# Performance work log

Hardware: AMD Instinct MI355X
Metric: run time of the kernel (lower is better)

Reference implementation:

```python
import jax, jax.numpy as jnp
import numpy as np

D_MODEL = 1024
NHEAD = 16
HEAD_DIM = D_MODEL // NHEAD
LN_EPS = 1e-5
ROPE_BASE = 10000.0


def _rope_cos_sin(n, head_dim):
    inv_freq = 1.0 / (ROPE_BASE ** (jnp.arange(0, head_dim, 2, dtype=jnp.float32) / head_dim))
    t = jnp.arange(n, dtype=jnp.float32)
    freqs = jnp.outer(t, inv_freq)  # (N, head_dim//2)
    return jnp.cos(freqs), jnp.sin(freqs)


def _apply_rope(x, cos, sin):
    # x: (B, H, N, hd); cos/sin: (N, hd//2)
    B, H, N, hd = x.shape
    xr = x.reshape(B, H, N, hd // 2, 2)
    x0, x1 = xr[..., 0], xr[..., 1]
    c = cos[None, None]
    s = sin[None, None]
    rot = jnp.stack([x0 * c - x1 * s, x0 * s + x1 * c], axis=-1)
    return rot.reshape(B, H, N, hd)


def setup_inputs() -> dict:
    key = jax.random.key(0)
    ks = jax.random.split(key, 6)
    D = D_MODEL
    scale = 1.0 / np.sqrt(D)
    x = jax.random.normal(ks[0], (2, 2048, D), dtype=jnp.float32)
    Wq = jax.random.normal(ks[1], (D, D), dtype=jnp.float32) * scale
    Wk = jax.random.normal(ks[2], (D, D), dtype=jnp.float32) * scale
    Wv = jax.random.normal(ks[3], (D, D), dtype=jnp.float32) * scale
    Wo = jax.random.normal(ks[4], (D, D), dtype=jnp.float32) * scale
    bq = jnp.zeros((D,), jnp.float32)
    bk = jnp.zeros((D,), jnp.float32)
    bv = jnp.zeros((D,), jnp.float32)
    bo = jnp.zeros((D,), jnp.float32)
    ln_w = jnp.ones((D,), jnp.float32)
    ln_b = jnp.zeros((D,), jnp.float32)
    return {"x": x, "ln_w": ln_w, "ln_b": ln_b, "Wq": Wq, "bq": bq,
            "Wk": Wk, "bk": bk, "Wv": Wv, "bv": bv, "Wo": Wo, "bo": bo}


def reference(x, ln_w, ln_b, Wq, bq, Wk, bk, Wv, bv, Wo, bo):
    B, N, D = x.shape
    H, hd = NHEAD, HEAD_DIM
    # LayerNorm
    mu = jnp.mean(x, axis=-1, keepdims=True)
    var = jnp.mean(jnp.square(x - mu), axis=-1, keepdims=True)
    xn = (x - mu) * jax.lax.rsqrt(var + LN_EPS) * ln_w + ln_b
    # QKV projections -> (B, H, N, hd)
    def proj(W, b):
        return (xn @ W.T + b).reshape(B, N, H, hd).transpose(0, 2, 1, 3)
    q = proj(Wq, bq)
    k = proj(Wk, bk)
    v = proj(Wv, bv)
    cos, sin = _rope_cos_sin(N, hd)
    q = _apply_rope(q, cos, sin)
    k = _apply_rope(k, cos, sin)
    scores = jnp.einsum('bhqd,bhkd->bhqk', q, k) / jnp.sqrt(jnp.float32(hd))
    attn = jax.nn.softmax(scores, axis=-1)
    out = jnp.einsum('bhqk,bhkd->bhqd', attn, v)
    out = out.transpose(0, 2, 1, 3).reshape(B, N, D)
    return x + out @ Wo.T + bo
```

## Files before the change

### kernel.cpp

```cpp
#include <hip/hip_runtime.h>


#define SEQ 2048
#define LN_EPS 1e-5f

using short8 = __attribute__((ext_vector_type(8))) short;
using f32x4  = __attribute__((ext_vector_type(4))) float;

__device__ __forceinline__ unsigned short f2bf(float f) {
  union { float f; unsigned u; } v; v.f = f;
  unsigned r = v.u + 0x7FFFu + ((v.u >> 16) & 1u);
  return (unsigned short)(r >> 16);
}

__device__ __forceinline__ void async16(const void* g, void* l) {
  __builtin_amdgcn_global_load_lds(
      (const __attribute__((address_space(1))) void*)g,
      (__attribute__((address_space(3))) void*)l, 16, 0, 0);
}

__global__ __launch_bounds__(256) void prep_kernel(
    const float* __restrict__ x, const float* __restrict__ lnw, const float* __restrict__ lnb,
    const float* __restrict__ wq, const float* __restrict__ wk,
    const float* __restrict__ wv, const float* __restrict__ wo,
    unsigned short* __restrict__ wqkv, unsigned short* __restrict__ wob,
    unsigned short* __restrict__ xn, float2* __restrict__ tab) {
  const int b = blockIdx.x, t = threadIdx.x;
  if (b < 4096) {
    const int gid = b * 256 + t;
    const int m = gid >> 18, e4 = gid & 262143;
    const float* src = (m == 0) ? wq : (m == 1) ? wk : (m == 2) ? wv : wo;
    const float4 v = ((const float4*)src)[e4];
    ushort4 o; o.x = f2bf(v.x); o.y = f2bf(v.y); o.z = f2bf(v.z); o.w = f2bf(v.w);
    if (m < 3) ((ushort4*)wqkv)[(size_t)m * 262144 + e4] = o;
    else       ((ushort4*)wob)[e4] = o;
  } else if (b < 8192) {
    const int row = b - 4096;
    const float4 v = ((const float4*)(x + (size_t)row * 1024))[t];
    float s  = v.x + v.y + v.z + v.w;
    float s2 = v.x * v.x + v.y * v.y + v.z * v.z + v.w * v.w;
#pragma unroll
    for (int off = 32; off >= 1; off >>= 1) {
      s  += __shfl_xor(s, off);
      s2 += __shfl_xor(s2, off);
    }
    __shared__ float red[8];
    const int lane = t & 63, wave = t >> 6;
    if (lane == 0) { red[wave] = s; red[4 + wave] = s2; }
    __syncthreads();
    s  = red[0] + red[1] + red[2] + red[3];
    s2 = red[4] + red[5] + red[6] + red[7];
    const float mu   = s * (1.0f / 1024.0f);
    const float var  = s2 * (1.0f / 1024.0f) - mu * mu;
    const float rstd = rsqrtf(var + LN_EPS);
    const float4 wv4 = ((const float4*)lnw)[t];
    const float4 bv4 = ((const float4*)lnb)[t];
    ushort4 o;
    o.x = f2bf((v.x - mu) * rstd * wv4.x + bv4.x);
    o.y = f2bf((v.y - mu) * rstd * wv4.y + bv4.y);
    o.z = f2bf((v.z - mu) * rstd * wv4.z + bv4.z);
    o.w = f2bf((v.w - mu) * rstd * wv4.w + bv4.w);
    ((ushort4*)xn)[(size_t)row * 256 + t] = o;
  } else {
    const int gid = (b - 8192) * 256 + t;
    const int pos = gid >> 5, ip = gid & 31;
    const float invf = exp2f((float)ip * -0.4152410118609203f);
    const float fr = (float)pos * invf;
    tab[gid] = make_float2(cosf(fr), sinf(fr));
  }
}

__global__ __launch_bounds__(256, 3) void gemm_qkv_kernel(
    const unsigned short* __restrict__ A,
    const unsigned short* __restrict__ Bw,
    const float* __restrict__ bq, const float* __restrict__ bk, const float* __restrict__ bv,
    const float2* __restrict__ tab,
    unsigned short* __restrict__ qb, unsigned short* __restrict__ kbg,
    unsigned short* __restrict__ vtb) {
  __shared__ unsigned short lA[128 * 64];
  __shared__ unsigned short lB[128 * 64];
  const int tid = threadIdx.x;
  const int lane = tid & 63, wave = tid >> 6;
  const int lr = lane & 15, quad = lane >> 4;
  const int wm = (wave >> 1) * 64, wn = (wave & 1) * 64;
  const int n0 = blockIdx.x * 128, m0 = blockIdx.y * 128;
  const int r7 = lr & 7;
  const int lrow = lane >> 3, lcg = (lane & 7) ^ lrow;
  const int lin = blockIdx.y * gridDim.x + blockIdx.x;
  const int phase = ((lin >> 8) * 5) & 15;

  f32x4 acc[4][4];
#pragma unroll
  for (int i = 0; i < 4; ++i)
#pragma unroll
    for (int j = 0; j < 4; ++j) acc[i][j] = (f32x4){0.f, 0.f, 0.f, 0.f};

  for (int kt = 0; kt < 16; ++kt) {
    const int kofs = ((kt + phase) & 15) * 64;
    __syncthreads();
#pragma unroll
    for (int c = 0; c < 4; ++c) {
      const int chunk = wave * 4 + c;
      const int grow = chunk * 8 + lrow;
      async16(&A[(size_t)(m0 + grow) * 1024 + kofs + lcg * 8], &lA[chunk * 512]);
      async16(&Bw[(size_t)(n0 + grow) * 1024 + kofs + lcg * 8], &lB[chunk * 512]);
    }
    __syncthreads();
#pragma unroll
    for (int kk = 0; kk < 2; ++kk) {
      short8 a[4], b[4];
#pragma unroll
      for (int i = 0; i < 4; ++i)
        a[i] = *(const short8*)&lA[(wm + i * 16 + lr) * 64 + ((kk * 4 + quad) ^ r7) * 8];
#pragma unroll
      for (int j = 0; j < 4; ++j)
        b[j] = *(const short8*)&lB[(wn + j * 16 + lr) * 64 + ((kk * 4 + quad) ^ r7) * 8];
#pragma unroll
      for (int i = 0; i < 4; ++i)
#pragma unroll
        for (int j = 0; j < 4; ++j)
          acc[i][j] = __builtin_amdgcn_mfma_f32_16x16x32_bf16(a[i], b[j], acc[i][j], 0, 0, 0);
    }
  }

  const int which = n0 >> 10;
  const float* bias = (which == 0) ? bq : (which == 1) ? bk : bv;
  const float qs = (which == 0) ? 0.18033688011112042f : 1.0f;
#pragma unroll
  for (int i = 0; i < 4; ++i)
#pragma unroll
    for (int j = 0; j < 4; ++j)
#pragma unroll
      for (int r = 0; r < 4; ++r) {
        const int row = m0 + wm + i * 16 + quad * 4 + r;
        const int col = n0 + wn + j * 16 + lr;
        const int c = col & 1023;
        float val = (acc[i][j][r] + bias[c]) * qs;
        const int head = c >> 6, hd_i = c & 63;
        const int b_ = row >> 11, pos = row & 2047;
        if (which < 2) {
          const float partner = __shfl_xor(val, 1);
          const float2 cs = tab[(pos << 5) + (hd_i >> 1)];
          val = val * cs.x + partner * ((lane & 1) ? cs.y : -cs.y);
        }
        if (which == 2) {
          vtb[((size_t)((b_ * 16 + head) * 64 + hd_i)) * SEQ + pos] = f2bf(val);
        } else {
          const size_t didx = ((size_t)((b_ * 16 + head) * SEQ + pos)) * 64 + hd_i;
          if (which == 0) qb[didx] = f2bf(val);
          else            kbg[didx] = f2bf(val);
        }
      }
}

__global__ __launch_bounds__(256, 3) void gemm_o_kernel(
    const unsigned short* __restrict__ A,
    const unsigned short* __restrict__ Bw,
    const float* __restrict__ bo, const float* __restrict__ xres, float* __restrict__ out) {
  __shared__ unsigned short lA[128 * 64];
  __shared__ unsigned short lB[64 * 64];
  const int tid = threadIdx.x;
  const int lane = tid & 63, wave = tid >> 6;
  const int lr = lane & 15, quad = lane >> 4;
  const int wm = (wave >> 1) * 64, wn = (wave & 1) * 32;
  const int n0 = blockIdx.x * 64, m0 = blockIdx.y * 128;
  const int r7 = lr & 7;
  const int lrow = lane >> 3, lcg = (lane & 7) ^ lrow;
  const int lin = blockIdx.y * gridDim.x + blockIdx.x;
  const int phase = ((lin >> 8) * 8) & 15;

  f32x4 acc[4][2];
#pragma unroll
  for (int i = 0; i < 4; ++i)
#pragma unroll
    for (int j = 0; j < 2; ++j) acc[i][j] = (f32x4){0.f, 0.f, 0.f, 0.f};

  for (int kt = 0; kt < 16; ++kt) {
    const int kofs = ((kt + phase) & 15) * 64;
    __syncthreads();
#pragma unroll
    for (int c = 0; c < 4; ++c) {
      const int chunk = wave * 4 + c;
      const int grow = chunk * 8 + lrow;
      async16(&A[(size_t)(m0 + grow) * 1024 + kofs + lcg * 8], &lA[chunk * 512]);
    }
#pragma unroll
    for (int c = 0; c < 2; ++c) {
      const int chunk = wave * 2 + c;
      const int grow = chunk * 8 + lrow;
      async16(&Bw[(size_t)(n0 + grow) * 1024 + kofs + lcg * 8], &lB[chunk * 512]);
    }
    __syncthreads();
#pragma unroll
    for (int kk = 0; kk < 2; ++kk) {
      short8 a[4], b[2];
#pragma unroll
      for (int i = 0; i < 4; ++i)
        a[i] = *(const short8*)&lA[(wm + i * 16 + lr) * 64 + ((kk * 4 + quad) ^ r7) * 8];
#pragma unroll
      for (int j = 0; j < 2; ++j)
        b[j] = *(const short8*)&lB[(wn + j * 16 + lr) * 64 + ((kk * 4 + quad) ^ r7) * 8];
#pragma unroll
      for (int i = 0; i < 4; ++i)
#pragma unroll
        for (int j = 0; j < 2; ++j)
          acc[i][j] = __builtin_amdgcn_mfma_f32_16x16x32_bf16(a[i], b[j], acc[i][j], 0, 0, 0);
    }
  }

#pragma unroll
  for (int i = 0; i < 4; ++i)
#pragma unroll
    for (int j = 0; j < 2; ++j)
#pragma unroll
      for (int r = 0; r < 4; ++r) {
        const int row = m0 + wm + i * 16 + quad * 4 + r;
        const int col = n0 + wn + j * 16 + lr;
        const size_t idx = (size_t)row * 1024 + col;
        out[idx] = acc[i][j][r] + bo[col] + xres[idx];
      }
}

__global__ __launch_bounds__(256) void attn_kernel(
    const unsigned short* __restrict__ qg, const unsigned short* __restrict__ kg,
    const unsigned short* __restrict__ vtg, unsigned short* __restrict__ ao) {
  __shared__ unsigned short lK[128 * 64];
  __shared__ unsigned short lV[64 * 128];
  __shared__ unsigned short lP[4][32 * 128];
  const int tid = threadIdx.x;
  const int lane = tid & 63, w = tid >> 6;
  const int lr = lane & 15, quad = lane >> 4;
  const int r7 = lr & 7;
  const int bh = blockIdx.x >> 4, qt = blockIdx.x & 15;
  const int q0 = qt * 128 + w * 32;
  const int phase = ((blockIdx.x >> 8) * 8) & 15;
  const unsigned short* Q  = qg + (size_t)bh * SEQ * 64;
  const unsigned short* K  = kg + (size_t)bh * SEQ * 64;
  const unsigned short* VT = vtg + (size_t)bh * 64 * SEQ;
  unsigned short* lPw = lP[w];

  short8 qf[2][2];
#pragma unroll
  for (int t = 0; t < 2; ++t)
#pragma unroll
    for (int kk = 0; kk < 2; ++kk)
      qf[t][kk] = *(const short8*)&Q[(size_t)(q0 + t * 16 + lr) * 64 + kk * 32 + quad * 8];

  short8 onesf;
  {
    const short o1 = (lr == 0) ? (short)0x3F80 : (short)0;
#pragma unroll
    for (int j = 0; j < 8; ++j) onesf[j] = o1;
  }

  f32x4 o[2][4], ol[2];
#pragma unroll
  for (int t = 0; t < 2; ++t) {
    ol[t] = (f32x4){0.f, 0.f, 0.f, 0.f};
#pragma unroll
    for (int d = 0; d < 4; ++d) o[t][d] = (f32x4){0.f, 0.f, 0.f, 0.f};
  }

  const int k_row = lane >> 3, k_g = (lane & 7) ^ (k_row & 7);
  const int v_row = lane >> 4, v_g0 = lane & 15;

  for (int kt = 0; kt < 16; ++kt) {
    const int kb0 = ((kt + phase) & 15) * 128;
    __syncthreads();
#pragma unroll
    for (int c = 0; c < 4; ++c) {
      const int kc = w * 4 + c;
      const int krow = kc * 8 + k_row;
      async16(&K[(size_t)(kb0 + krow) * 64 + k_g * 8], &lK[kc * 512]);
      const int vc = w * 4 + c;
      const int vrow = vc * 4 + v_row;
      const int vg = v_g0 ^ (vrow & 7);
      async16(&VT[(size_t)vrow * SEQ + kb0 + vg * 8], &lV[vc * 512]);
    }
    __syncthreads();

#pragma unroll
    for (int kb = 0; kb < 8; ++kb) {
      const short8 k0 = *(const short8*)&lK[(kb * 16 + lr) * 64 + (quad ^ r7) * 8];
      const short8 k1 = *(const short8*)&lK[(kb * 16 + lr) * 64 + ((4 + quad) ^ r7) * 8];
#pragma unroll
      for (int t = 0; t < 2; ++t) {
        f32x4 st = (f32x4){0.f, 0.f, 0.f, 0.f};
        st = __builtin_amdgcn_mfma_f32_16x16x32_bf16(k0, qf[t][0], st, 0, 0, 0);
        st = __builtin_amdgcn_mfma_f32_16x16x32_bf16(k1, qf[t][1], st, 0, 0, 0);
        union { float f; unsigned u; } c0, c1, c2, c3;
        c0.f = __builtin_amdgcn_exp2f(st[0]);
        c1.f = __builtin_amdgcn_exp2f(st[1]);
        c2.f = __builtin_amdgcn_exp2f(st[2]);
        c3.f = __builtin_amdgcn_exp2f(st[3]);
        uint2 pw;
        pw.x = __builtin_amdgcn_perm(c1.u, c0.u, 0x07060302u);
        pw.y = __builtin_amdgcn_perm(c3.u, c2.u, 0x07060302u);
        *(uint2*)&lPw[(t * 16 + lr) * 128 + ((kb * 2 + (quad >> 1)) ^ r7) * 8 + (quad & 1) * 4] = pw;
      }
    }
    __asm__ __volatile__("s_waitcnt lgkmcnt(0)" ::: "memory");

#pragma unroll
    for (int k2 = 0; k2 < 4; ++k2) {
      const short8 pf0 = *(const short8*)&lPw[lr * 128 + ((k2 * 4 + quad) ^ r7) * 8];
      const short8 pf1 = *(const short8*)&lPw[(16 + lr) * 128 + ((k2 * 4 + quad) ^ r7) * 8];
      ol[0] = __builtin_amdgcn_mfma_f32_16x16x32_bf16(pf0, onesf, ol[0], 0, 0, 0);
      ol[1] = __builtin_amdgcn_mfma_f32_16x16x32_bf16(pf1, onesf, ol[1], 0, 0, 0);
#pragma unroll
      for (int d = 0; d < 4; ++d) {
        const short8 vf = *(const short8*)&lV[(d * 16 + lr) * 128 + ((k2 * 4 + quad) ^ r7) * 8];
        o[0][d] = __builtin_amdgcn_mfma_f32_16x16x32_bf16(pf0, vf, o[0][d], 0, 0, 0);
        o[1][d] = __builtin_amdgcn_mfma_f32_16x16x32_bf16(pf1, vf, o[1][d], 0, 0, 0);
      }
    }
  }

  const int b_ = bh >> 4, h = bh & 15;
#pragma unroll
  for (int t = 0; t < 2; ++t)
#pragma unroll
    for (int r = 0; r < 4; ++r) {
      const float l = __shfl(ol[t][r], lane & 48);
      const float rl = 1.0f / l;
#pragma unroll
      for (int d = 0; d < 4; ++d) {
        const int row = q0 + t * 16 + quad * 4 + r;
        ao[(size_t)(b_ * SEQ + row) * 1024 + h * 64 + d * 16 + lr] = f2bf(o[t][d][r] * rl);
      }
    }
}

extern "C" void kernel_launch(void* const* d_in, const int* in_sizes, int n_in,
                              void* d_out, int out_size, void* d_ws, size_t ws_size,
                              hipStream_t stream) {
  const float* x   = (const float*)d_in[0];
  const float* lnw = (const float*)d_in[1];
  const float* lnb = (const float*)d_in[2];
  const float* Wq  = (const float*)d_in[3];
  const float* bq  = (const float*)d_in[4];
  const float* Wk  = (const float*)d_in[5];
  const float* bk  = (const float*)d_in[6];
  const float* Wv  = (const float*)d_in[7];
  const float* bv  = (const float*)d_in[8];
  const float* Wo  = (const float*)d_in[9];
  const float* bo  = (const float*)d_in[10];
  float* out = (float*)d_out;

  char* ws = (char*)d_ws;
  unsigned short* wqkv = (unsigned short*)(ws);
  unsigned short* wob  = (unsigned short*)(ws + 6291456);
  unsigned short* xn   = (unsigned short*)(ws + 8388608);
  unsigned short* qb   = (unsigned short*)(ws + 16777216);
  unsigned short* kbuf = (unsigned short*)(ws + 25165824);
  unsigned short* vtb  = (unsigned short*)(ws + 33554432);
  unsigned short* ao   = (unsigned short*)(ws + 41943040);
  float2*         tab  = (float2*)(ws + 50331648);

  hipLaunchKernelGGL(prep_kernel, dim3(8448), dim3(256), 0, stream,
                     x, lnw, lnb, Wq, Wk, Wv, Wo, wqkv, wob, xn, tab);
  hipLaunchKernelGGL(gemm_qkv_kernel, dim3(24, 32), dim3(256), 0, stream,
                     xn, wqkv, bq, bk, bv, tab, qb, kbuf, vtb);
  hipLaunchKernelGGL(attn_kernel, dim3(512), dim3(256), 0, stream, qb, kbuf, vtb, ao);
  hipLaunchKernelGGL(gemm_o_kernel, dim3(16, 32), dim3(256), 0, stream,
                     ao, wob, bo, x, out);
}
```

Before: 220.8 us.

## Rewrite attention with 32x32 MFMA, register-resident P, and double-buffered K/V

The attention kernel moves from 16x16x32 to 32x32x16 bf16 MFMA tiles. Probabilities stay in registers, rearranged with permlane32_swap, instead of round-tripping through per-wave LDS. The row sum is accumulated with scalar adds rather than a ones-vector MFMA. K/V tiles are double-buffered so the next tile's async loads overlap compute, which drops one barrier per iteration. This doubles the K/V LDS footprint and adds cross-lane shuffles, and correctness depends on matching the 32x32 accumulator layout.

Result: no change. 223.9 us (+1.4%).

```diff
diff --git a/kernel.cpp b/kernel.cpp
--- a/kernel.cpp
+++ b/kernel.cpp
@@ -6,6 +6,7 @@
 
 using short8 = __attribute__((ext_vector_type(8))) short;
 using f32x4  = __attribute__((ext_vector_type(4))) float;
+using f32x16 = __attribute__((ext_vector_type(16))) float;
 
 __device__ __forceinline__ unsigned short f2bf(float f) {
   union { float f; unsigned u; } v; v.f = f;
@@ -224,111 +225,125 @@
 __global__ __launch_bounds__(256) void attn_kernel(
     const unsigned short* __restrict__ qg, const unsigned short* __restrict__ kg,
     const unsigned short* __restrict__ vtg, unsigned short* __restrict__ ao) {
-  __shared__ unsigned short lK[128 * 64];
-  __shared__ unsigned short lV[64 * 128];
-  __shared__ unsigned short lP[4][32 * 128];
+  __shared__ unsigned short lK[2][128 * 64];
+  __shared__ unsigned short lV[2][64 * 128];
   const int tid = threadIdx.x;
   const int lane = tid & 63, w = tid >> 6;
-  const int lr = lane & 15, quad = lane >> 4;
-  const int r7 = lr & 7;
+  const int l31 = lane & 31, hb = lane >> 5, l7 = lane & 7;
   const int bh = blockIdx.x >> 4, qt = blockIdx.x & 15;
-  const int q0 = qt * 128 + w * 32;
+  const int q0w = qt * 128 + w * 32;
   const int phase = ((blockIdx.x >> 8) * 8) & 15;
   const unsigned short* Q  = qg + (size_t)bh * SEQ * 64;
   const unsigned short* K  = kg + (size_t)bh * SEQ * 64;
   const unsigned short* VT = vtg + (size_t)bh * 64 * SEQ;
-  unsigned short* lPw = lP[w];
-
-  short8 qf[2][2];
-#pragma unroll
-  for (int t = 0; t < 2; ++t)
-#pragma unroll
-    for (int kk = 0; kk < 2; ++kk)
-      qf[t][kk] = *(const short8*)&Q[(size_t)(q0 + t * 16 + lr) * 64 + kk * 32 + quad * 8];
-
-  short8 onesf;
-  {
-    const short o1 = (lr == 0) ? (short)0x3F80 : (short)0;
-#pragma unroll
-    for (int j = 0; j < 8; ++j) onesf[j] = o1;
-  }
-
-  f32x4 o[2][4], ol[2];
-#pragma unroll
-  for (int t = 0; t < 2; ++t) {
-    ol[t] = (f32x4){0.f, 0.f, 0.f, 0.f};
-#pragma unroll
-    for (int d = 0; d < 4; ++d) o[t][d] = (f32x4){0.f, 0.f, 0.f, 0.f};
-  }
+
+  short8 qf[4];
+#pragma unroll
+  for (int c = 0; c < 4; ++c)
+    qf[c] = *(const short8*)&Q[(size_t)(q0w + l31) * 64 + c * 16 + hb * 8];
+
+  f32x16 o[2];
+#pragma unroll
+  for (int dh = 0; dh < 2; ++dh)
+#pragma unroll
+    for (int r = 0; r < 16; ++r) o[dh][r] = 0.f;
+  float ls = 0.f;
 
   const int k_row = lane >> 3, k_g = (lane & 7) ^ (k_row & 7);
   const int v_row = lane >> 4, v_g0 = lane & 15;
 
-  for (int kt = 0; kt < 16; ++kt) {
-    const int kb0 = ((kt + phase) & 15) * 128;
-    __syncthreads();
+  {
+    const int kb0 = (phase & 15) * 128;
 #pragma unroll
     for (int c = 0; c < 4; ++c) {
       const int kc = w * 4 + c;
       const int krow = kc * 8 + k_row;
-      async16(&K[(size_t)(kb0 + krow) * 64 + k_g * 8], &lK[kc * 512]);
-      const int vc = w * 4 + c;
-      const int vrow = vc * 4 + v_row;
+      async16(&K[(size_t)(kb0 + krow) * 64 + k_g * 8], &lK[0][kc * 512]);
+      const int vrow = kc * 4 + v_row;
       const int vg = v_g0 ^ (vrow & 7);
-      async16(&VT[(size_t)vrow * SEQ + kb0 + vg * 8], &lV[vc * 512]);
-    }
-    __syncthreads();
-
-#pragma unroll
-    for (int kb = 0; kb < 8; ++kb) {
-      const short8 k0 = *(const short8*)&lK[(kb * 16 + lr) * 64 + (quad ^ r7) * 8];
-      const short8 k1 = *(const short8*)&lK[(kb * 16 + lr) * 64 + ((4 + quad) ^ r7) * 8];
-#pragma unroll
-      for (int t = 0; t < 2; ++t) {
-        f32x4 st = (f32x4){0.f, 0.f, 0.f, 0.f};
-        st = __builtin_amdgcn_mfma_f32_16x16x32_bf16(k0, qf[t][0], st, 0, 0, 0);
-        st = __builtin_amdgcn_mfma_f32_16x16x32_bf16(k1, qf[t][1], st, 0, 0, 0);
-        union { float f; unsigned u; } c0, c1, c2, c3;
-        c0.f = __builtin_amdgcn_exp2f(st[0]);
-        c1.f = __builtin_amdgcn_exp2f(st[1]);
-        c2.f = __builtin_amdgcn_exp2f(st[2]);
-        c3.f = __builtin_amdgcn_exp2f(st[3]);
-        uint2 pw;
-        pw.x = __builtin_amdgcn_perm(c1.u, c0.u, 0x07060302u);
-        pw.y = __builtin_amdgcn_perm(c3.u, c2.u, 0x07060302u);
-        *(uint2*)&lPw[(t * 16 + lr) * 128 + ((kb * 2 + (quad >> 1)) ^ r7) * 8 + (quad & 1) * 4] = pw;
-      }
-    }
-    __asm__ __volatile__("s_waitcnt lgkmcnt(0)" ::: "memory");
-
-#pragma unroll
-    for (int k2 = 0; k2 < 4; ++k2) {
-      const short8 pf0 = *(const short8*)&lPw[lr * 128 + ((k2 * 4 + quad) ^ r7) * 8];
-      const short8 pf1 = *(const short8*)&lPw[(16 + lr) * 128 + ((k2 * 4 + quad) ^ r7) * 8];
-      ol[0] = __builtin_amdgcn_mfma_f32_16x16x32_bf16(pf0, onesf, ol[0], 0, 0, 0);
-      ol[1] = __builtin_amdgcn_mfma_f32_16x16x32_bf16(pf1, onesf, ol[1], 0, 0, 0);
-#pragma unroll
-      for (int d = 0; d < 4; ++d) {
-        const short8 vf = *(const short8*)&lV[(d * 16 + lr) * 128 + ((k2 * 4 + quad) ^ r7) * 8];
-        o[0][d] = __builtin_amdgcn_mfma_f32_16x16x32_bf16(pf0, vf, o[0][d], 0, 0, 0);
-        o[1][d] = __builtin_amdgcn_mfma_f32_16x16x32_bf16(pf1, vf, o[1][d], 0, 0, 0);
-      }
-    }
-  }
+      async16(&VT[(size_t)vrow * SEQ + kb0 + vg * 8], &lV[0][kc * 512]);
+    }
+  }
+  __syncthreads();
+
+  for (int kt = 0; kt < 16; ++kt) {
+    const int cur = kt & 1;
+    if (kt < 15) {
+      const int kb0 = ((kt + 1 + phase) & 15) * 128;
+#pragma unroll
+      for (int c = 0; c < 4; ++c) {
+        const int kc = w * 4 + c;
+        const int krow = kc * 8 + k_row;
+        async16(&K[(size_t)(kb0 + krow) * 64 + k_g * 8], &lK[cur ^ 1][kc * 512]);
+        const int vrow = kc * 4 + v_row;
+        const int vg = v_g0 ^ (vrow & 7);
+        async16(&VT[(size_t)vrow * SEQ + kb0 + vg * 8], &lV[cur ^ 1][kc * 512]);
+      }
+    }
+    const unsigned short* Kb = lK[cur];
+    const unsigned short* Vb = lV[cur];
+
+#pragma unroll
+    for (int kb2 = 0; kb2 < 4; ++kb2) {
+      f32x16 sv;
+#pragma unroll
+      for (int r = 0; r < 16; ++r) sv[r] = 0.f;
+      const int key = kb2 * 32 + l31;
+#pragma unroll
+      for (int c = 0; c < 4; ++c) {
+        const short8 af = *(const short8*)&Kb[key * 64 + (((c * 2 + hb) ^ l7) << 3)];
+        sv = __builtin_amdgcn_mfma_f32_32x32x16_bf16(af, qf[c], sv, 0, 0, 0);
+      }
+      unsigned wp[8];
+#pragma unroll
+      for (int p = 0; p < 8; ++p) {
+        union { float f; unsigned u; } e0, e1;
+        e0.f = __builtin_amdgcn_exp2f(sv[2 * p]);
+        e1.f = __builtin_amdgcn_exp2f(sv[2 * p + 1]);
+        ls += e0.f + e1.f;
+        wp[p] = __builtin_amdgcn_perm(e1.u, e0.u, 0x07060302u);
+      }
+      unsigned wlo[8], whi[8];
+#pragma unroll
+      for (int p = 0; p < 8; ++p) {
+        auto rr = __builtin_amdgcn_permlane32_swap(wp[p], wp[p], false, false);
+        wlo[p] = rr[0]; whi[p] = rr[1];
+      }
+#pragma unroll
+      for (int cl = 0; cl < 2; ++cl) {
+        const int pb = cl * 4;
+        union { unsigned u[4]; short8 s; } pf;
+        pf.u[0] = hb ? wlo[pb + 2] : wlo[pb + 0];
+        pf.u[1] = hb ? wlo[pb + 3] : wlo[pb + 1];
+        pf.u[2] = hb ? whi[pb + 2] : whi[pb + 0];
+        pf.u[3] = hb ? whi[pb + 3] : whi[pb + 1];
+        const int chunk = kb2 * 2 + cl;
+#pragma unroll
+        for (int dh = 0; dh < 2; ++dh) {
+          const int d = dh * 32 + l31;
+          const short8 vf = *(const short8*)&Vb[d * 128 + (((chunk * 2 + hb) ^ l7) << 3)];
+          o[dh] = __builtin_amdgcn_mfma_f32_32x32x16_bf16(pf.s, vf, o[dh], 0, 0, 0);
+        }
+      }
+    }
+    __syncthreads();
+  }
+
+  union { float f; unsigned u; } lsu; lsu.f = ls;
+  auto lr2 = __builtin_amdgcn_permlane32_swap(lsu.u, lsu.u, false, false);
+  union { unsigned u; float f; } la, lb2; la.u = lr2[0]; lb2.u = lr2[1];
+  const float rl = 1.0f / (la.f + lb2.f);
 
   const int b_ = bh >> 4, h = bh & 15;
 #pragma unroll
-  for (int t = 0; t < 2; ++t)
-#pragma unroll
-    for (int r = 0; r < 4; ++r) {
-      const float l = __shfl(ol[t][r], lane & 48);
-      const float rl = 1.0f / l;
-#pragma unroll
-      for (int d = 0; d < 4; ++d) {
-        const int row = q0 + t * 16 + quad * 4 + r;
-        ao[(size_t)(b_ * SEQ + row) * 1024 + h * 64 + d * 16 + lr] = f2bf(o[t][d][r] * rl);
-      }
-    }
+  for (int r = 0; r < 16; ++r) {
+    const int m = (r & 3) + 8 * (r >> 2) + 4 * hb;
+    const float rlv = __shfl(rl, m);
+    const int row = q0w + m;
+#pragma unroll
+    for (int dh = 0; dh < 2; ++dh)
+      ao[(size_t)(b_ * SEQ + row) * 1024 + h * 64 + dh * 32 + l31] = f2bf(o[dh][r] * rlv);
+  }
 }
 
 extern "C" void kernel_launch(void* const* d_in, const int* in_sizes, int n_in,
```
